# Kernel tuning notes

Hardware: AMD Instinct MI355X
Metric: run time of the kernel (lower is better)

Reference implementation:

```python
import jax, jax.numpy as jnp
import numpy as np

B, T, H, POOL, MAX_ITER = 32, 1024, 128, 16, 4
D = 2 * H  # feature size of U rows


def _maxout(x, w, b, out_dim, pool):
    # x: [..., fin], w: [fin, out_dim*pool], b: [out_dim*pool]
    y = x @ w + b
    y = y.reshape(y.shape[:-1] + (out_dim, pool))
    return y.max(axis=-1)


def _hmn(U, us, ue, h, WDw, WDb, W1w, W1b, W2w, W2b, W3w, W3b):
    # U: [B,T,2H]; us, ue: [B,2H]; h: [B,H] -> scores [B,T]
    r = jnp.tanh(jnp.concatenate([h, us, ue], axis=-1) @ WDw + WDb)  # [B,H]
    rt = jnp.broadcast_to(r[:, None, :], (U.shape[0], U.shape[1], r.shape[-1]))
    m1 = _maxout(jnp.concatenate([U, rt], axis=-1), W1w, W1b, H, POOL)  # [B,T,H]
    m2 = _maxout(m1, W2w, W2b, H, POOL)                                  # [B,T,H]
    m3 = _maxout(jnp.concatenate([m1, m2], axis=-1), W3w, W3b, 1, POOL)  # [B,T,1]
    return m3[..., 0]  # [B,T]


def _lstm_cell(x, h, c, wih, whh, bih, bhh):
    gates = x @ wih.T + bih + h @ whh.T + bhh  # [B,4H]
    i, f, g, o = jnp.split(gates, 4, axis=-1)
    i, f, o = jax.nn.sigmoid(i), jax.nn.sigmoid(f), jax.nn.sigmoid(o)
    g = jnp.tanh(g)
    c2 = f * c + i * g
    h2 = o * jnp.tanh(c2)
    return h2, c2


def setup_inputs() -> dict:
    key = jax.random.key(0)
    ks = jax.random.split(key, 24)
    s = 0.05
    gn = lambda k, shape: (jax.random.normal(k, shape, jnp.float32) * s)
    inp = {"U": jax.random.normal(ks[0], (B, T, D), jnp.float32)}
    for tag, off in (("s", 1), ("e", 9)):
        inp[f"WD{tag}_w"] = gn(ks[off + 0], (5 * H, H))
        inp[f"WD{tag}_b"] = jnp.zeros((H,), jnp.float32)
        inp[f"W1{tag}_w"] = gn(ks[off + 1], (3 * H, H * POOL))
        inp[f"W1{tag}_b"] = jnp.zeros((H * POOL,), jnp.float32)
        inp[f"W2{tag}_w"] = gn(ks[off + 2], (H, H * POOL))
        inp[f"W2{tag}_b"] = jnp.zeros((H * POOL,), jnp.float32)
        inp[f"W3{tag}_w"] = gn(ks[off + 3], (2 * H, POOL))
        inp[f"W3{tag}_b"] = jnp.zeros((POOL,), jnp.float32)
    inp["lstm_wih"] = gn(ks[20], (4 * H, 4 * H))
    inp["lstm_whh"] = gn(ks[21], (4 * H, H))
    inp["lstm_bih"] = jnp.zeros((4 * H,), jnp.float32)
    inp["lstm_bhh"] = jnp.zeros((4 * H,), jnp.float32)
    return inp


def reference(U,
              WDs_w, WDs_b, W1s_w, W1s_b, W2s_w, W2s_b, W3s_w, W3s_b,
              WDe_w, WDe_b, W1e_w, W1e_b, W2e_w, W2e_b, W3e_w, W3e_b,
              lstm_wih, lstm_whh, lstm_bih, lstm_bhh):
    b = U.shape[0]
    bidx = jnp.arange(b)
    h = jnp.zeros((b, H), U.dtype)
    c = jnp.zeros((b, H), U.dtype)
    us, ue = U[:, 0, :], U[:, 1, :]
    entropies = []
    for _ in range(MAX_ITER):  # training-mode: run all iterations (no host-sync early stop)
        alpha_sc = _hmn(U, us, ue, h, WDs_w, WDs_b, W1s_w, W1s_b, W2s_w, W2s_b, W3s_w, W3s_b)
        alpha = jnp.argmax(alpha_sc, axis=1)           # [B]
        us = U[bidx, alpha, :]                          # data-dependent gather
        beta_sc = _hmn(U, us, ue, h, WDe_w, WDe_b, W1e_w, W1e_b, W2e_w, W2e_b, W3e_w, W3e_b)
        beta = jnp.argmax(beta_sc, axis=1)
        ue = U[bidx, beta, :]
        h, c = _lstm_cell(jnp.concatenate([us, ue], axis=1), h, c,
                          lstm_wih, lstm_whh, lstm_bih, lstm_bhh)
        entropies.append(jnp.stack([alpha_sc, beta_sc], axis=0))
    ent = jnp.stack(entropies, axis=0)  # [max_iter, 2, B, T]
    return alpha, beta, ent
```

## Files before the change

### kernel.cpp

```cpp
#include <hip/hip_runtime.h>
#include <math.h>

static constexpr int cB = 32;
static constexpr int cT = 1024;
static constexpr int cH = 128;
static constexpr int cD = 256;
static constexpr int cN = 2048;
static constexpr int cM = cB * cT;

typedef __attribute__((ext_vector_type(8))) short short8;
typedef __attribute__((ext_vector_type(4))) float f32x4;

__device__ __forceinline__ ushort f2bf(float x) {
    union { float f; unsigned u; } v; v.f = x;
    unsigned r = v.u + 0x7FFF + ((v.u >> 16) & 1);
    return (ushort)(r >> 16);
}
__device__ __forceinline__ float bf2f(ushort h) {
    union { float f; unsigned u; } v; v.u = ((unsigned)h) << 16;
    return v.f;
}

__device__ __forceinline__ void gload_lds16(const ushort* g, ushort* l) {
    __builtin_amdgcn_global_load_lds(
        (const __attribute__((address_space(1))) unsigned int*)(const void*)g,
        (__attribute__((address_space(3))) unsigned int*)(void*)l,
        16, 0, 0);
}

template<int K, bool WRITE_HL>
__global__ __launch_bounds__(256, 2)
void mfma_pool_swp(const ushort* __restrict__ Wth, const ushort* __restrict__ Wtl,
                   const ushort* __restrict__ Xh, const ushort* __restrict__ Xl,
                   const float* __restrict__ initv, int init_bstride,
                   float* __restrict__ out, ushort* __restrict__ outh,
                   ushort* __restrict__ outl)
{
    constexpr int KH = K / 128;
    __shared__ __attribute__((aligned(16))) ushort sWh[128 * 128];
    __shared__ __attribute__((aligned(16))) ushort sWl[128 * 128];

    const int tid  = threadIdx.x;
    const int wave = tid >> 6;
    const int lane = tid & 63;
    const int l15  = lane & 15;
    const int lg   = lane >> 4;
    const int wr   = wave >> 1;
    const int wc   = wave & 1;

    const int wg  = blockIdx.x;
    const int lin = (wg & 7) * 512 + (wg >> 3);
    const int bx  = lin & 15;
    const int by  = lin >> 4;
    const int n0  = bx * 128;
    const int m0  = by * 128;
    const size_t ibase = (size_t)(m0 >> 10) * init_bstride;

    float ivv[4][4];
    #pragma unroll
    for (int rf = 0; rf < 4; ++rf)
        #pragma unroll
        for (int r = 0; r < 4; ++r)
            ivv[rf][r] = initv[ibase + n0 + wr * 64 + rf * 16 + lg * 4 + r];

    f32x4 acc[4][4];
    #pragma unroll
    for (int rf = 0; rf < 4; ++rf)
        #pragma unroll
        for (int cf = 0; cf < 4; ++cf)
            acc[rf][cf] = (f32x4){0.f, 0.f, 0.f, 0.f};

    const int st_row_lo = lane >> 4;
    const int st_slot   = lane & 15;

    #pragma unroll
    for (int kh = 0; kh < KH; ++kh) {
        const int kb = kh * 128;
        if (kh > 0) __syncthreads();

        #pragma unroll
        for (int j = 0; j < 8; ++j) {
            int i   = wave * 8 + j;
            int row = i * 4 + st_row_lo;
            int ck  = st_slot ^ (row & 7);
            size_t goff = (size_t)(n0 + row) * K + kb + ck * 8;
            gload_lds16(Wth + goff, sWh + i * 512);
            gload_lds16(Wtl + goff, sWl + i * 512);
        }
        short8 xh_[16], xl_[16];
        #pragma unroll
        for (int cf = 0; cf < 4; ++cf)
            #pragma unroll
            for (int ks = 0; ks < 4; ++ks) {
                size_t off = (size_t)(m0 + wc * 64 + cf * 16 + l15) * K
                           + kb + ks * 32 + lg * 8;
                xh_[cf * 4 + ks] = *(const short8*)(Xh + off);
                xl_[cf * 4 + ks] = *(const short8*)(Xl + off);
            }
        __syncthreads();

        #pragma unroll
        for (int ks = 0; ks < 4; ++ks) {
            short8 w_h[4], w_l[4];
            #pragma unroll
            for (int rf = 0; rf < 4; ++rf) {
                int row  = wr * 64 + rf * 16 + l15;
                int ck2  = ks * 4 + lg;
                int adr  = row * 128 + ((ck2 ^ (row & 7)) * 8);
                w_h[rf] = *(const short8*)(sWh + adr);
                w_l[rf] = *(const short8*)(sWl + adr);
            }
            #pragma unroll
            for (int rf = 0; rf < 4; ++rf)
                #pragma unroll
                for (int cf = 0; cf < 4; ++cf) {
                    acc[rf][cf] = __builtin_amdgcn_mfma_f32_16x16x32_bf16(
                        w_h[rf], xh_[cf * 4 + ks], acc[rf][cf], 0, 0, 0);
                    acc[rf][cf] = __builtin_amdgcn_mfma_f32_16x16x32_bf16(
                        w_l[rf], xh_[cf * 4 + ks], acc[rf][cf], 0, 0, 0);
                    acc[rf][cf] = __builtin_amdgcn_mfma_f32_16x16x32_bf16(
                        w_h[rf], xl_[cf * 4 + ks], acc[rf][cf], 0, 0, 0);
                }
        }
    }

    const int NP = 128;
    #pragma unroll
    for (int rf = 0; rf < 4; ++rf) {
        const int o2 = (n0 >> 4) + wr * 4 + rf;
        #pragma unroll
        for (int cf = 0; cf < 4; ++cf) {
            float v0 = acc[rf][cf][0] + ivv[rf][0];
            float v1 = acc[rf][cf][1] + ivv[rf][1];
            float v2 = acc[rf][cf][2] + ivv[rf][2];
            float v3 = acc[rf][cf][3] + ivv[rf][3];
            float mx = fmaxf(fmaxf(v0, v1), fmaxf(v2, v3));
            mx = fmaxf(mx, __shfl_xor(mx, 16));
            mx = fmaxf(mx, __shfl_xor(mx, 32));
            if (lane < 16) {
                int m = m0 + wc * 64 + cf * 16 + lane;
                size_t o = (size_t)m * NP + o2;
                out[o] = mx;
                if (WRITE_HL) {
                    ushort hb = f2bf(mx);
                    outh[o] = hb;
                    outl[o] = f2bf(mx - bf2f(hb));
                }
            }
        }
    }
}

__global__ __launch_bounds__(256, 2)
void mfma_gemm_a1(const ushort* __restrict__ Uh, const ushort* __restrict__ Ul,
                  const ushort* __restrict__ Bth, const ushort* __restrict__ Btl,
                  float* __restrict__ out)
{
    constexpr int K = 256;
    __shared__ __attribute__((aligned(16))) ushort sBh[128 * 128];
    __shared__ __attribute__((aligned(16))) ushort sBl[128 * 128];

    const int tid  = threadIdx.x;
    const int wave = tid >> 6;
    const int lane = tid & 63;
    const int l15  = lane & 15;
    const int lg   = lane >> 4;
    const int wr   = wave >> 1;
    const int wc   = wave & 1;

    const int wg  = blockIdx.x;
    const int lin = (wg & 7) * 512 + (wg >> 3);
    const int bx  = lin & 15;
    const int by  = lin >> 4;
    const int n0  = bx * 128;
    const int m0  = by * 128;

    f32x4 acc[4][4];
    #pragma unroll
    for (int mf = 0; mf < 4; ++mf)
        #pragma unroll
        for (int nf = 0; nf < 4; ++nf)
            acc[mf][nf] = (f32x4){0.f, 0.f, 0.f, 0.f};

    const int st_row_lo = lane >> 4;
    const int st_slot   = lane & 15;

    #pragma unroll
    for (int kh = 0; kh < 2; ++kh) {
        const int kb = kh * 128;
        if (kh > 0) __syncthreads();

        #pragma unroll
        for (int j = 0; j < 8; ++j) {
            int i   = wave * 8 + j;
            int row = i * 4 + st_row_lo;
            int ck  = st_slot ^ (row & 7);
            size_t goff = (size_t)(n0 + row) * K + kb + ck * 8;
            gload_lds16(Bth + goff, sBh + i * 512);
            gload_lds16(Btl + goff, sBl + i * 512);
        }
        short8 ph[16], pl[16];
        #pragma unroll
        for (int mf = 0; mf < 4; ++mf)
            #pragma unroll
            for (int ks = 0; ks < 4; ++ks) {
                size_t off = (size_t)(m0 + wr * 64 + mf * 16 + l15) * K
                           + kb + ks * 32 + lg * 8;
                ph[mf * 4 + ks] = *(const short8*)(Uh + off);
                pl[mf * 4 + ks] = *(const short8*)(Ul + off);
            }
        __syncthreads();

        #pragma unroll
        for (int ks = 0; ks < 4; ++ks) {
            short8 b_h[4], b_l[4];
            #pragma unroll
            for (int nf = 0; nf < 4; ++nf) {
                int row  = wc * 64 + nf * 16 + l15;
                int ck2  = ks * 4 + lg;
                int adr  = row * 128 + ((ck2 ^ (row & 7)) * 8);
                b_h[nf] = *(const short8*)(sBh + adr);
                b_l[nf] = *(const short8*)(sBl + adr);
            }
            #pragma unroll
            for (int mf = 0; mf < 4; ++mf)
                #pragma unroll
                for (int nf = 0; nf < 4; ++nf) {
                    acc[mf][nf] = __builtin_amdgcn_mfma_f32_16x16x32_bf16(
                        ph[mf * 4 + ks], b_h[nf], acc[mf][nf], 0, 0, 0);
                    acc[mf][nf] = __builtin_amdgcn_mfma_f32_16x16x32_bf16(
                        ph[mf * 4 + ks], b_l[nf], acc[mf][nf], 0, 0, 0);
                    acc[mf][nf] = __builtin_amdgcn_mfma_f32_16x16x32_bf16(
                        pl[mf * 4 + ks], b_h[nf], acc[mf][nf], 0, 0, 0);
                }
        }
    }

    #pragma unroll
    for (int mf = 0; mf < 4; ++mf)
        #pragma unroll
        for (int nf = 0; nf < 4; ++nf) {
            int col = n0 + wc * 64 + nf * 16 + l15;
            #pragma unroll
            for (int r = 0; r < 4; ++r) {
                int row = m0 + wr * 64 + mf * 16 + lg * 4 + r;
                out[(size_t)row * cN + col] = acc[mf][nf][r];
            }
        }
}

__global__ void m1_from_a1_kernel(const float* __restrict__ A1,
                                  const float* __restrict__ rterm,
                                  float* __restrict__ m1,
                                  ushort* __restrict__ m1h,
                                  ushort* __restrict__ m1l)
{
    int idx = blockIdx.x * 256 + threadIdx.x;
    int m = idx >> 7;
    int o = idx & 127;
    int b = m >> 10;
    const float4* a  = (const float4*)(A1 + (size_t)m * cN + o * 16);
    const float4* rt = (const float4*)(rterm + (size_t)b * cN + o * 16);
    float mx = -3.4e38f;
    #pragma unroll
    for (int q = 0; q < 4; ++q) {
        float4 av = a[q];
        float4 rv = rt[q];
        mx = fmaxf(mx, fmaxf(fmaxf(av.x + rv.x, av.y + rv.y),
                             fmaxf(av.z + rv.z, av.w + rv.w)));
    }
    m1[idx] = mx;
    ushort hb = f2bf(mx);
    m1h[idx] = hb;
    m1l[idx] = f2bf(mx - bf2f(hb));
}

__global__ void wsplit_kernel(const float* __restrict__ W, int K, int N,
                              ushort* __restrict__ th, ushort* __restrict__ tl)
{
    int idx = blockIdx.x * 256 + threadIdx.x;
    if (idx >= K * N) return;
    int k = idx / N, n = idx - k * N;
    float x = W[idx];
    ushort h = f2bf(x);
    th[(size_t)n * K + k] = h;
    tl[(size_t)n * K + k] = f2bf(x - bf2f(h));
}

__global__ void usplit_kernel(const float* __restrict__ U,
                              ushort* __restrict__ uh, ushort* __restrict__ ul)
{
    int idx = blockIdx.x * 256 + threadIdx.x;
    float x = U[idx];
    ushort h = f2bf(x);
    uh[idx] = h;
    ul[idx] = f2bf(x - bf2f(h));
}

__global__ void r_kernel(const float* __restrict__ h, const float* __restrict__ us,
                         const float* __restrict__ ue,
                         const float* __restrict__ WDw, const float* __restrict__ WDb,
                         float* __restrict__ r)
{
    int b = blockIdx.x;
    int j = threadIdx.x;
    __shared__ float x[640];
    x[j]       = h[b * cH + j];
    x[128 + j] = us[b * cD + j];
    x[256 + j] = us[b * cD + 128 + j];
    x[384 + j] = ue[b * cD + j];
    x[512 + j] = ue[b * cD + 128 + j];
    __syncthreads();
    float s = WDb[j];
    for (int k = 0; k < 640; ++k) s = fmaf(x[k], WDw[(size_t)k * cH + j], s);
    r[b * cH + j] = tanhf(s);
}

__global__ void rterm_kernel(const float* __restrict__ r, const float* __restrict__ W1r,
                             const float* __restrict__ W1b, float* __restrict__ rterm)
{
    int b = blockIdx.y;
    int n = blockIdx.x * 256 + threadIdx.x;
    __shared__ float rs[128];
    if (threadIdx.x < 128) rs[threadIdx.x] = r[b * cH + threadIdx.x];
    __syncthreads();
    float s = W1b[n];
    for (int k = 0; k < 128; ++k) s = fmaf(rs[k], W1r[(size_t)k * cN + n], s);
    rterm[(size_t)b * cN + n] = s;
}

__global__ __launch_bounds__(256)
void score_kernel(const float* __restrict__ m1, const float* __restrict__ m2,
                  const float* __restrict__ W3w, const float* __restrict__ W3b,
                  float* __restrict__ ent)
{
    __shared__ float xs[16][257];
    __shared__ float wsh[256 * 16];
    int tid = threadIdx.x;
    int m0 = blockIdx.x * 16;
    #pragma unroll
    for (int q = 0; q < 16; ++q) wsh[tid + q * 256] = W3w[tid + q * 256];
    #pragma unroll
    for (int q = 0; q < 8; ++q) {
        int f = tid + q * 256;
        int rl = f >> 7, col = f & 127;
        xs[rl][col]       = m1[(size_t)(m0 + rl) * cH + col];
        xs[rl][128 + col] = m2[(size_t)(m0 + rl) * cH + col];
    }
    __syncthreads();
    int rl = tid >> 4, p = tid & 15;
    float s = W3b[p];
    for (int k = 0; k < 256; ++k) s = fmaf(xs[rl][k], wsh[k * 16 + p], s);
    #pragma unroll
    for (int off = 8; off; off >>= 1) s = fmaxf(s, __shfl_xor(s, off));
    if (p == 0) ent[m0 + rl] = s;
}

__global__ void argmax_kernel(const float* __restrict__ sc, const float* __restrict__ U,
                              float* __restrict__ uvec, float* __restrict__ outidx)
{
    int b = blockIdx.x;
    int tid = threadIdx.x;
    float bv = -3.4e38f;
    int bi = 0x7fffffff;
    for (int t = tid; t < cT; t += 256) {
        float v = sc[b * cT + t];
        if (v > bv || (v == bv && t < bi)) { bv = v; bi = t; }
    }
    __shared__ float vs[256];
    __shared__ int   is[256];
    vs[tid] = bv; is[tid] = bi;
    __syncthreads();
    for (int s = 128; s > 0; s >>= 1) {
        if (tid < s) {
            if (vs[tid + s] > vs[tid] ||
                (vs[tid + s] == vs[tid] && is[tid + s] < is[tid])) {
                vs[tid] = vs[tid + s];
                is[tid] = is[tid + s];
            }
        }
        __syncthreads();
    }
    int best = is[0];
    if (tid == 0) outidx[b] = (float)best;
    uvec[b * cD + tid % cD] = U[((size_t)b * cT + best) * cD + (tid % cD)];
}

__global__ void lstm_kernel(const float* __restrict__ us, const float* __restrict__ ue,
                            float* __restrict__ h, float* __restrict__ c,
                            const float* __restrict__ wih, const float* __restrict__ whh,
                            const float* __restrict__ bih, const float* __restrict__ bhh)
{
    int b = blockIdx.x;
    int j = threadIdx.x;
    __shared__ float x[512];
    __shared__ float hh[128];
    x[j]       = us[b * cD + j];
    x[128 + j] = us[b * cD + 128 + j];
    x[256 + j] = ue[b * cD + j];
    x[384 + j] = ue[b * cD + 128 + j];
    hh[j] = h[b * cH + j];
    __syncthreads();
    float g4[4];
    #pragma unroll
    for (int gi = 0; gi < 4; ++gi) {
        int row = gi * 128 + j;
        float s = bih[row] + bhh[row];
        const float* wr = wih + (size_t)row * 512;
        for (int k = 0; k < 512; ++k) s = fmaf(x[k], wr[k], s);
        const float* wr2 = whh + (size_t)row * 128;
        for (int k = 0; k < 128; ++k) s = fmaf(hh[k], wr2[k], s);
        g4[gi] = s;
    }
    float i_ = 1.f / (1.f + expf(-g4[0]));
    float f_ = 1.f / (1.f + expf(-g4[1]));
    float g_ = tanhf(g4[2]);
    float o_ = 1.f / (1.f + expf(-g4[3]));
    float c2 = f_ * c[b * cH + j] + i_ * g_;
    float h2 = o_ * tanhf(c2);
    c[b * cH + j] = c2;
    h[b * cH + j] = h2;
}

__global__ void init_kernel(const float* __restrict__ U, float* __restrict__ us,
                            float* __restrict__ ue, float* __restrict__ h,
                            float* __restrict__ c)
{
    int i = blockIdx.x * 256 + threadIdx.x;
    if (i < cB * cD) {
        int b = i >> 8, d = i & 255;
        us[i] = U[((size_t)b * cT + 0) * cD + d];
        ue[i] = U[((size_t)b * cT + 1) * cD + d];
    }
    if (i < cB * cH) { h[i] = 0.f; c[i] = 0.f; }
}

extern "C" void kernel_launch(void* const* d_in, const int* in_sizes, int n_in,
                              void* d_out, int out_size, void* d_ws, size_t ws_size,
                              hipStream_t stream)
{
    const float* U = (const float*)d_in[0];
    const float* WD_w[2] = {(const float*)d_in[1], (const float*)d_in[9]};
    const float* WD_b[2] = {(const float*)d_in[2], (const float*)d_in[10]};
    const float* W1_w[2] = {(const float*)d_in[3], (const float*)d_in[11]};
    const float* W1_b[2] = {(const float*)d_in[4], (const float*)d_in[12]};
    const float* W2_w[2] = {(const float*)d_in[5], (const float*)d_in[13]};
    const float* W2_b[2] = {(const float*)d_in[6], (const float*)d_in[14]};
    const float* W3_w[2] = {(const float*)d_in[7], (const float*)d_in[15]};
    const float* W3_b[2] = {(const float*)d_in[8], (const float*)d_in[16]};
    const float* wih = (const float*)d_in[17];
    const float* whh = (const float*)d_in[18];
    const float* bih = (const float*)d_in[19];
    const float* bhh = (const float*)d_in[20];

    float* ws = (float*)d_ws;
    float* m1 = ws;
    float* m2 = m1 + (size_t)cM * cH;
    float* us = m2 + (size_t)cM * cH;
    float* ue = us + cB * cD;
    float* h  = ue + cB * cD;
    float* c  = h + cB * cH;
    float* r  = c + cB * cH;
    float* rterm = r + cB * cH;
    float* cur = rterm + (size_t)cB * cN;

    ushort* m1h = (ushort*)cur;                   cur += (size_t)cM * cH / 2;
    ushort* m1l = (ushort*)cur;                   cur += (size_t)cM * cH / 2;
    ushort* Uh  = (ushort*)cur;                   cur += (size_t)cM * cD / 2;
    ushort* Ul  = (ushort*)cur;                   cur += (size_t)cM * cD / 2;
    ushort* W1th[2], *W1tl[2], *W2th[2], *W2tl[2];
    for (int sd = 0; sd < 2; ++sd) {
        W1th[sd] = (ushort*)cur; cur += (size_t)cN * cD / 2;
        W1tl[sd] = (ushort*)cur; cur += (size_t)cN * cD / 2;
        W2th[sd] = (ushort*)cur; cur += (size_t)cN * cH / 2;
        W2tl[sd] = (ushort*)cur; cur += (size_t)cN * cH / 2;
    }
    float* A1[2];
    A1[0] = cur;
    A1[1] = A1[0] + (size_t)cM * cN;
    size_t need = (size_t)(A1[1] - ws) + (size_t)cM * cN;
    bool pre = ws_size >= need * sizeof(float);

    float* outf = (float*)d_out;

    init_kernel<<<32, 256, 0, stream>>>(U, us, ue, h, c);
    usplit_kernel<<<(cM * cD) / 256, 256, 0, stream>>>(U, Uh, Ul);
    for (int sd = 0; sd < 2; ++sd) {
        wsplit_kernel<<<(cD * cN) / 256, 256, 0, stream>>>(
            W1_w[sd], cD, cN, W1th[sd], W1tl[sd]);
        wsplit_kernel<<<(cH * cN) / 256, 256, 0, stream>>>(
            W2_w[sd], cH, cN, W2th[sd], W2tl[sd]);
    }

    const int ggrid = (cN / 128) * (cM / 128);
    if (pre) {
        for (int sd = 0; sd < 2; ++sd)
            mfma_gemm_a1<<<ggrid, 256, 0, stream>>>(
                Uh, Ul, W1th[sd], W1tl[sd], A1[sd]);
    }

    for (int it = 0; it < 4; ++it) {
        for (int sd = 0; sd < 2; ++sd) {
            r_kernel<<<32, 128, 0, stream>>>(h, us, ue, WD_w[sd], WD_b[sd], r);
            rterm_kernel<<<dim3(8, 32), 256, 0, stream>>>(
                r, W1_w[sd] + (size_t)256 * cN, W1_b[sd], rterm);
            if (pre) {
                m1_from_a1_kernel<<<16384, 256, 0, stream>>>(
                    A1[sd], rterm, m1, m1h, m1l);
            } else {
                mfma_pool_swp<256, true><<<ggrid, 256, 0, stream>>>(
                    W1th[sd], W1tl[sd], Uh, Ul, rterm, cN, m1, m1h, m1l);
            }
            mfma_pool_swp<128, false><<<ggrid, 256, 0, stream>>>(
                W2th[sd], W2tl[sd], m1h, m1l, W2_b[sd], 0, m2, nullptr, nullptr);
            float* ent = outf + 64 + (size_t)(it * 2 + sd) * cB * cT;
            score_kernel<<<2048, 256, 0, stream>>>(m1, m2, W3_w[sd], W3_b[sd], ent);
            argmax_kernel<<<32, 256, 0, stream>>>(ent, U, sd ? ue : us,
                                                  outf + (sd ? 32 : 0));
        }
        lstm_kernel<<<32, 128, 0, stream>>>(us, ue, h, c, wih, whh, bih, bhh);
    }
}
```

Baseline: 2.868 ms.

## Use weight-stationary persistent MFMA kernels for A1 precompute and W2 maxout GEMM

Replaces the LDS-staged A1 GEMM and the per-iteration W2 maxout GEMM with weight-stationary kernels. Each workgroup keeps its slice of the split bf16 weights in registers and loops over many M sub-tiles, streaming activations straight from global memory. The grid shrinks to 256 workgroups, which removes repeated LDS staging of the weights and the syncs around it. In exchange it raises register pressure (launch bounds 1), gives less parallelism and latency hiding, and loads activations without LDS reuse across waves.

```diff
diff --git a/kernel.cpp b/kernel.cpp
--- a/kernel.cpp
+++ b/kernel.cpp
@@ -26,6 +26,179 @@
         (const __attribute__((address_space(1))) unsigned int*)(const void*)g,
         (__attribute__((address_space(3))) unsigned int*)(void*)l,
         16, 0, 0);
+}
+
+__global__ __launch_bounds__(256, 1)
+void mfma_pool_ws(const ushort* __restrict__ Wth, const ushort* __restrict__ Wtl,
+                  const ushort* __restrict__ Xh, const ushort* __restrict__ Xl,
+                  const float* __restrict__ bias, float* __restrict__ out)
+{
+    constexpr int K = 128;
+    const int lane = threadIdx.x & 63;
+    const int wave = threadIdx.x >> 6;
+    const int l15  = lane & 15;
+    const int lg   = lane >> 4;
+    const int wr   = wave >> 1;
+    const int wc   = wave & 1;
+
+    const int wg  = blockIdx.x;
+    const int lin = (wg & 7) * 32 + (wg >> 3);
+    const int bx  = lin & 15;
+    const int by  = lin >> 4;
+    const int n0  = bx * 128;
+    const int mg0 = by * 2048;
+
+    short8 w_h[4][4], w_l[4][4];
+    #pragma unroll
+    for (int rf = 0; rf < 4; ++rf)
+        #pragma unroll
+        for (int ks = 0; ks < 4; ++ks) {
+            size_t off = (size_t)(n0 + wr * 64 + rf * 16 + l15) * K
+                       + ks * 32 + lg * 8;
+            w_h[rf][ks] = *(const short8*)(Wth + off);
+            w_l[rf][ks] = *(const short8*)(Wtl + off);
+        }
+    float ivv[4][4];
+    #pragma unroll
+    for (int rf = 0; rf < 4; ++rf)
+        #pragma unroll
+        for (int r = 0; r < 4; ++r)
+            ivv[rf][r] = bias[n0 + wr * 64 + rf * 16 + lg * 4 + r];
+
+    const int NP = 128;
+    #pragma unroll 1
+    for (int sub = 0; sub < 16; ++sub) {
+        const int m0 = mg0 + sub * 128;
+
+        short8 xh_[4][4], xl_[4][4];
+        #pragma unroll
+        for (int cf = 0; cf < 4; ++cf)
+            #pragma unroll
+            for (int ks = 0; ks < 4; ++ks) {
+                size_t off = (size_t)(m0 + wc * 64 + cf * 16 + l15) * K
+                           + ks * 32 + lg * 8;
+                xh_[cf][ks] = *(const short8*)(Xh + off);
+                xl_[cf][ks] = *(const short8*)(Xl + off);
+            }
+
+        f32x4 acc[4][4];
+        #pragma unroll
+        for (int rf = 0; rf < 4; ++rf)
+            #pragma unroll
+            for (int cf = 0; cf < 4; ++cf)
+                acc[rf][cf] = (f32x4){0.f, 0.f, 0.f, 0.f};
+
+        #pragma unroll
+        for (int ks = 0; ks < 4; ++ks)
+            #pragma unroll
+            for (int rf = 0; rf < 4; ++rf)
+                #pragma unroll
+                for (int cf = 0; cf < 4; ++cf) {
+                    acc[rf][cf] = __builtin_amdgcn_mfma_f32_16x16x32_bf16(
+                        w_h[rf][ks], xh_[cf][ks], acc[rf][cf], 0, 0, 0);
+                    acc[rf][cf] = __builtin_amdgcn_mfma_f32_16x16x32_bf16(
+                        w_l[rf][ks], xh_[cf][ks], acc[rf][cf], 0, 0, 0);
+                    acc[rf][cf] = __builtin_amdgcn_mfma_f32_16x16x32_bf16(
+                        w_h[rf][ks], xl_[cf][ks], acc[rf][cf], 0, 0, 0);
+                }
+
+        #pragma unroll
+        for (int rf = 0; rf < 4; ++rf) {
+            const int o2 = (n0 >> 4) + wr * 4 + rf;
+            #pragma unroll
+            for (int cf = 0; cf < 4; ++cf) {
+                float v0 = acc[rf][cf][0] + ivv[rf][0];
+                float v1 = acc[rf][cf][1] + ivv[rf][1];
+                float v2 = acc[rf][cf][2] + ivv[rf][2];
+                float v3 = acc[rf][cf][3] + ivv[rf][3];
+                float mx = fmaxf(fmaxf(v0, v1), fmaxf(v2, v3));
+                mx = fmaxf(mx, __shfl_xor(mx, 16));
+                mx = fmaxf(mx, __shfl_xor(mx, 32));
+                if (lane < 16) {
+                    int m = m0 + wc * 64 + cf * 16 + lane;
+                    out[(size_t)m * NP + o2] = mx;
+                }
+            }
+        }
+    }
+}
+
+__global__ __launch_bounds__(256, 1)
+void mfma_a1_ws(const ushort* __restrict__ Uh, const ushort* __restrict__ Ul,
+                const ushort* __restrict__ Bth, const ushort* __restrict__ Btl,
+                float* __restrict__ out)
+{
+    constexpr int K = 256;
+    const int lane = threadIdx.x & 63;
+    const int wave = threadIdx.x >> 6;
+    const int l15  = lane & 15;
+    const int lg   = lane >> 4;
+    const int wr   = wave >> 1;
+    const int wc   = wave & 1;
+
+    const int wg  = blockIdx.x;
+    const int lin = (wg & 7) * 32 + (wg >> 3);
+    const int bx  = lin & 31;
+    const int by  = lin >> 5;
+    const int n0  = bx * 64;
+    const int mg0 = by * 4096;
+
+    short8 b_h[2][8], b_l[2][8];
+    #pragma unroll
+    for (int nf = 0; nf < 2; ++nf)
+        #pragma unroll
+        for (int ks = 0; ks < 8; ++ks) {
+            size_t off = (size_t)(n0 + wc * 32 + nf * 16 + l15) * K
+                       + ks * 32 + lg * 8;
+            b_h[nf][ks] = *(const short8*)(Bth + off);
+            b_l[nf][ks] = *(const short8*)(Btl + off);
+        }
+
+    #pragma unroll 1
+    for (int sub = 0; sub < 32; ++sub) {
+        const int m0 = mg0 + sub * 128;
+        f32x4 acc[4][2];
+        #pragma unroll
+        for (int mf = 0; mf < 4; ++mf)
+            #pragma unroll
+            for (int nf = 0; nf < 2; ++nf)
+                acc[mf][nf] = (f32x4){0.f, 0.f, 0.f, 0.f};
+
+        #pragma unroll
+        for (int mf = 0; mf < 4; ++mf) {
+            short8 uh_[8], ul_[8];
+            #pragma unroll
+            for (int ks = 0; ks < 8; ++ks) {
+                size_t off = (size_t)(m0 + wr * 64 + mf * 16 + l15) * K
+                           + ks * 32 + lg * 8;
+                uh_[ks] = *(const short8*)(Uh + off);
+                ul_[ks] = *(const short8*)(Ul + off);
+            }
+            #pragma unroll
+            for (int ks = 0; ks < 8; ++ks)
+                #pragma unroll
+                for (int nf = 0; nf < 2; ++nf) {
+                    acc[mf][nf] = __builtin_amdgcn_mfma_f32_16x16x32_bf16(
+                        uh_[ks], b_h[nf][ks], acc[mf][nf], 0, 0, 0);
+                    acc[mf][nf] = __builtin_amdgcn_mfma_f32_16x16x32_bf16(
+                        uh_[ks], b_l[nf][ks], acc[mf][nf], 0, 0, 0);
+                    acc[mf][nf] = __builtin_amdgcn_mfma_f32_16x16x32_bf16(
+                        ul_[ks], b_h[nf][ks], acc[mf][nf], 0, 0, 0);
+                }
+        }
+
+        #pragma unroll
+        for (int mf = 0; mf < 4; ++mf)
+            #pragma unroll
+            for (int nf = 0; nf < 2; ++nf) {
+                int col = n0 + wc * 32 + nf * 16 + l15;
+                #pragma unroll
+                for (int r = 0; r < 4; ++r) {
+                    int row = m0 + wr * 64 + mf * 16 + lg * 4 + r;
+                    out[(size_t)row * cN + col] = acc[mf][nf][r];
+                }
+            }
+    }
 }
 
 template<int K, bool WRITE_HL>
@@ -151,104 +324,6 @@
     }
 }
 
-__global__ __launch_bounds__(256, 2)
-void mfma_gemm_a1(const ushort* __restrict__ Uh, const ushort* __restrict__ Ul,
-                  const ushort* __restrict__ Bth, const ushort* __restrict__ Btl,
-                  float* __restrict__ out)
-{
-    constexpr int K = 256;
-    __shared__ __attribute__((aligned(16))) ushort sBh[128 * 128];
-    __shared__ __attribute__((aligned(16))) ushort sBl[128 * 128];
-
-    const int tid  = threadIdx.x;
-    const int wave = tid >> 6;
-    const int lane = tid & 63;
-    const int l15  = lane & 15;
-    const int lg   = lane >> 4;
-    const int wr   = wave >> 1;
-    const int wc   = wave & 1;
-
-    const int wg  = blockIdx.x;
-    const int lin = (wg & 7) * 512 + (wg >> 3);
-    const int bx  = lin & 15;
-    const int by  = lin >> 4;
-    const int n0  = bx * 128;
-    const int m0  = by * 128;
-
-    f32x4 acc[4][4];
-    #pragma unroll
-    for (int mf = 0; mf < 4; ++mf)
-        #pragma unroll
-        for (int nf = 0; nf < 4; ++nf)
-            acc[mf][nf] = (f32x4){0.f, 0.f, 0.f, 0.f};
-
-    const int st_row_lo = lane >> 4;
-    const int st_slot   = lane & 15;
-
-    #pragma unroll
-    for (int kh = 0; kh < 2; ++kh) {
-        const int kb = kh * 128;
-        if (kh > 0) __syncthreads();
-
-        #pragma unroll
-        for (int j = 0; j < 8; ++j) {
-            int i   = wave * 8 + j;
-            int row = i * 4 + st_row_lo;
-            int ck  = st_slot ^ (row & 7);
-            size_t goff = (size_t)(n0 + row) * K + kb + ck * 8;
-            gload_lds16(Bth + goff, sBh + i * 512);
-            gload_lds16(Btl + goff, sBl + i * 512);
-        }
-        short8 ph[16], pl[16];
-        #pragma unroll
-        for (int mf = 0; mf < 4; ++mf)
-            #pragma unroll
-            for (int ks = 0; ks < 4; ++ks) {
-                size_t off = (size_t)(m0 + wr * 64 + mf * 16 + l15) * K
-                           + kb + ks * 32 + lg * 8;
-                ph[mf * 4 + ks] = *(const short8*)(Uh + off);
-                pl[mf * 4 + ks] = *(const short8*)(Ul + off);
-            }
-        __syncthreads();
-
-        #pragma unroll
-        for (int ks = 0; ks < 4; ++ks) {
-            short8 b_h[4], b_l[4];
-            #pragma unroll
-            for (int nf = 0; nf < 4; ++nf) {
-                int row  = wc * 64 + nf * 16 + l15;
-                int ck2  = ks * 4 + lg;
-                int adr  = row * 128 + ((ck2 ^ (row & 7)) * 8);
-                b_h[nf] = *(const short8*)(sBh + adr);
-                b_l[nf] = *(const short8*)(sBl + adr);
-            }
-            #pragma unroll
-            for (int mf = 0; mf < 4; ++mf)
-                #pragma unroll
-                for (int nf = 0; nf < 4; ++nf) {
-                    acc[mf][nf] = __builtin_amdgcn_mfma_f32_16x16x32_bf16(
-                        ph[mf * 4 + ks], b_h[nf], acc[mf][nf], 0, 0, 0);
-                    acc[mf][nf] = __builtin_amdgcn_mfma_f32_16x16x32_bf16(
-                        ph[mf * 4 + ks], b_l[nf], acc[mf][nf], 0, 0, 0);
-                    acc[mf][nf] = __builtin_amdgcn_mfma_f32_16x16x32_bf16(
-                        pl[mf * 4 + ks], b_h[nf], acc[mf][nf], 0, 0, 0);
-                }
-        }
-    }
-
-    #pragma unroll
-    for (int mf = 0; mf < 4; ++mf)
-        #pragma unroll
-        for (int nf = 0; nf < 4; ++nf) {
-            int col = n0 + wc * 64 + nf * 16 + l15;
-            #pragma unroll
-            for (int r = 0; r < 4; ++r) {
-                int row = m0 + wr * 64 + mf * 16 + lg * 4 + r;
-                out[(size_t)row * cN + col] = acc[mf][nf][r];
-            }
-        }
-}
-
 __global__ void m1_from_a1_kernel(const float* __restrict__ A1,
                                   const float* __restrict__ rterm,
                                   float* __restrict__ m1,
@@ -492,13 +567,13 @@
             W2_w[sd], cH, cN, W2th[sd], W2tl[sd]);
     }
 
-    const int ggrid = (cN / 128) * (cM / 128);
     if (pre) {
         for (int sd = 0; sd < 2; ++sd)
-            mfma_gemm_a1<<<ggrid, 256, 0, stream>>>(
+            mfma_a1_ws<<<256, 256, 0, stream>>>(
                 Uh, Ul, W1th[sd], W1tl[sd], A1[sd]);
     }
 
+    const int gfall = (cN / 128) * (cM / 128);
     for (int it = 0; it < 4; ++it) {
         for (int sd = 0; sd < 2; ++sd) {
             r_kernel<<<32, 128, 0, stream>>>(h, us, ue, WD_w[sd], WD_b[sd], r);
@@ -508,11 +583,11 @@
                 m1_from_a1_kernel<<<16384, 256, 0, stream>>>(
                     A1[sd], rterm, m1, m1h, m1l);
             } else {
-                mfma_pool_swp<256, true><<<ggrid, 256, 0, stream>>>(
+                mfma_pool_swp<256, true><<<gfall, 256, 0, stream>>>(
                     W1th[sd], W1tl[sd], Uh, Ul, rterm, cN, m1, m1h, m1l);
             }
-            mfma_pool_swp<128, false><<<ggrid, 256, 0, stream>>>(
-                W2th[sd], W2tl[sd], m1h, m1l, W2_b[sd], 0, m2, nullptr, nullptr);
+            mfma_pool_ws<<<256, 256, 0, stream>>>(
+                W2th[sd], W2tl[sd], m1h, m1l, W2_b[sd], m2);
             float* ent = outf + 64 + (size_t)(it * 2 + sd) * cB * cT;
             score_kernel<<<2048, 256, 0, stream>>>(m1, m2, W3_w[sd], W3_b[sd], ent);
             argmax_kernel<<<32, 256, 0, stream>>>(ent, U, sd ? ue : us,
```

Measured after the change: 3.198 ms. 1.12x slower.

## Partially precompute A1 to fit workspace and persist W2 tiles across M blocks

Applied to the files above, without the earlier changes.

Replaces the all-or-nothing precompute of U@W1 with a split: as many rows as fit in the workspace are precomputed once, and the remainder run through the fused MFMA pool kernel at an M offset. Adds a dedicated m2 kernel that loads the W2 tile into LDS once and loops over four 128-row M blocks, cutting redundant weight staging and halving the grid. The m2 kernel also uses three MFMAs, dropping the low-low bf16 product, which slightly reduces precision.

```diff
diff --git a/kernel.cpp b/kernel.cpp
--- a/kernel.cpp
+++ b/kernel.cpp
@@ -28,15 +28,14 @@
         16, 0, 0);
 }
 
-template<int K, bool WRITE_HL>
 __global__ __launch_bounds__(256, 2)
 void mfma_pool_swp(const ushort* __restrict__ Wth, const ushort* __restrict__ Wtl,
                    const ushort* __restrict__ Xh, const ushort* __restrict__ Xl,
                    const float* __restrict__ initv, int init_bstride,
                    float* __restrict__ out, ushort* __restrict__ outh,
-                   ushort* __restrict__ outl)
-{
-    constexpr int KH = K / 128;
+                   ushort* __restrict__ outl, int mOff, int gridDiv8)
+{
+    constexpr int K = 256;
     __shared__ __attribute__((aligned(16))) ushort sWh[128 * 128];
     __shared__ __attribute__((aligned(16))) ushort sWl[128 * 128];
 
@@ -49,11 +48,11 @@
     const int wc   = wave & 1;
 
     const int wg  = blockIdx.x;
-    const int lin = (wg & 7) * 512 + (wg >> 3);
+    const int lin = (wg & 7) * gridDiv8 + (wg >> 3);
     const int bx  = lin & 15;
     const int by  = lin >> 4;
     const int n0  = bx * 128;
-    const int m0  = by * 128;
+    const int m0  = mOff + by * 128;
     const size_t ibase = (size_t)(m0 >> 10) * init_bstride;
 
     float ivv[4][4];
@@ -74,7 +73,7 @@
     const int st_slot   = lane & 15;
 
     #pragma unroll
-    for (int kh = 0; kh < KH; ++kh) {
+    for (int kh = 0; kh < 2; ++kh) {
         const int kb = kh * 128;
         if (kh > 0) __syncthreads();
 
@@ -141,11 +140,9 @@
                 int m = m0 + wc * 64 + cf * 16 + lane;
                 size_t o = (size_t)m * NP + o2;
                 out[o] = mx;
-                if (WRITE_HL) {
-                    ushort hb = f2bf(mx);
-                    outh[o] = hb;
-                    outl[o] = f2bf(mx - bf2f(hb));
-                }
+                ushort hb = f2bf(mx);
+                outh[o] = hb;
+                outl[o] = f2bf(mx - bf2f(hb));
             }
         }
     }
@@ -154,7 +151,7 @@
 __global__ __launch_bounds__(256, 2)
 void mfma_gemm_a1(const ushort* __restrict__ Uh, const ushort* __restrict__ Ul,
                   const ushort* __restrict__ Bth, const ushort* __restrict__ Btl,
-                  float* __restrict__ out)
+                  float* __restrict__ out, int gridDiv8)
 {
     constexpr int K = 256;
     __shared__ __attribute__((aligned(16))) ushort sBh[128 * 128];
@@ -169,7 +166,7 @@
     const int wc   = wave & 1;
 
     const int wg  = blockIdx.x;
-    const int lin = (wg & 7) * 512 + (wg >> 3);
+    const int lin = (wg & 7) * gridDiv8 + (wg >> 3);
     const int bx  = lin & 15;
     const int by  = lin >> 4;
     const int n0  = bx * 128;
@@ -273,6 +270,117 @@
     ushort hb = f2bf(mx);
     m1h[idx] = hb;
     m1l[idx] = f2bf(mx - bf2f(hb));
+}
+
+__global__ __launch_bounds__(256, 2)
+void mfma_pool_m2(const ushort* __restrict__ Wth, const ushort* __restrict__ Wtl,
+                  const ushort* __restrict__ Xh, const ushort* __restrict__ Xl,
+                  const float* __restrict__ bias, float* __restrict__ out)
+{
+    constexpr int K = 128;
+    __shared__ __attribute__((aligned(16))) ushort sWh[128 * 128];
+    __shared__ __attribute__((aligned(16))) ushort sWl[128 * 128];
+
+    const int tid  = threadIdx.x;
+    const int wave = tid >> 6;
+    const int lane = tid & 63;
+    const int l15  = lane & 15;
+    const int lg   = lane >> 4;
+    const int wr   = wave >> 1;
+    const int wc   = wave & 1;
+
+    const int wg  = blockIdx.x;
+    const int lin = (wg & 7) * 128 + (wg >> 3);
+    const int bx  = lin & 15;
+    const int by  = lin >> 4;
+    const int n0  = bx * 128;
+
+    float ivv[4][4];
+    #pragma unroll
+    for (int rf = 0; rf < 4; ++rf)
+        #pragma unroll
+        for (int r = 0; r < 4; ++r)
+            ivv[rf][r] = bias[n0 + wr * 64 + rf * 16 + lg * 4 + r];
+
+    const int st_row_lo = lane >> 4;
+    const int st_slot   = lane & 15;
+    #pragma unroll
+    for (int j = 0; j < 8; ++j) {
+        int i   = wave * 8 + j;
+        int row = i * 4 + st_row_lo;
+        int ck  = st_slot ^ (row & 7);
+        size_t goff = (size_t)(n0 + row) * K + ck * 8;
+        gload_lds16(Wth + goff, sWh + i * 512);
+        gload_lds16(Wtl + goff, sWl + i * 512);
+    }
+    __syncthreads();
+
+    const int NP = 128;
+    #pragma unroll 1
+    for (int s = 0; s < 4; ++s) {
+        const int m0 = by * 512 + s * 128;
+
+        short8 xh_[16], xl_[16];
+        #pragma unroll
+        for (int cf = 0; cf < 4; ++cf)
+            #pragma unroll
+            for (int ks = 0; ks < 4; ++ks) {
+                size_t off = (size_t)(m0 + wc * 64 + cf * 16 + l15) * K
+                           + ks * 32 + lg * 8;
+                xh_[cf * 4 + ks] = *(const short8*)(Xh + off);
+                xl_[cf * 4 + ks] = *(const short8*)(Xl + off);
+            }
+
+        f32x4 acc[4][4];
+        #pragma unroll
+        for (int rf = 0; rf < 4; ++rf)
+            #pragma unroll
+            for (int cf = 0; cf < 4; ++cf)
+                acc[rf][cf] = (f32x4){0.f, 0.f, 0.f, 0.f};
+
+        #pragma unroll
+        for (int ks = 0; ks < 4; ++ks) {
+            short8 w_h[4], w_l[4];
+            #pragma unroll
+            for (int rf = 0; rf < 4; ++rf) {
+                int row  = wr * 64 + rf * 16 + l15;
+                int ck2  = ks * 4 + lg;
+                int adr  = row * 128 + ((ck2 ^ (row & 7)) * 8);
+                w_h[rf] = *(const short8*)(sWh + adr);
+                w_l[rf] = *(const short8*)(sWl + adr);
+            }
+            #pragma unroll
+            for (int rf = 0; rf < 4; ++rf)
+                #pragma unroll
+                for (int cf = 0; cf < 4; ++cf) {
+                    acc[rf][cf] = __builtin_amdgcn_mfma_f32_16x16x32_bf16(
+                        w_h[rf], xh_[cf * 4 + ks], acc[rf][cf], 0, 0, 0);
+                    acc[rf][cf] = __builtin_amdgcn_mfma_f32_16x16x32_bf16(
+                        w_l[rf], xh_[cf * 4 + ks], acc[rf][cf], 0, 0, 0);
+                    acc[rf][cf] = __builtin_amdgcn_mfma_f32_16x16x32_bf16(
+                        w_h[rf], xl_[cf * 4 + ks], acc[rf][cf], 0, 0, 0);
+                }
+        }
+
+        #pragma unroll
+        for (int rf = 0; rf < 4; ++rf) {
+            const int o2 = (n0 >> 4) + wr * 4 + rf;
+            #pragma unroll
+            for (int cf = 0; cf < 4; ++cf) {
+                float v0 = acc[rf][cf][0] + ivv[rf][0];
+                float v1 = acc[rf][cf][1] + ivv[rf][1];
+                float v2 = acc[rf][cf][2] + ivv[rf][2];
+                float v3 = acc[rf][cf][3] + ivv[rf][3];
+                float mx = fmaxf(fmaxf(v0, v1), fmaxf(v2, v3));
+                mx = fmaxf(mx, __shfl_xor(mx, 16));
+                mx = fmaxf(mx, __shfl_xor(mx, 32));
+                if (lane < 16) {
+                    int m = m0 + wc * 64 + cf * 16 + lane;
+                    out[(size_t)m * NP + o2] = mx;
+                }
+            }
+        }
+    }
 }
 
 __global__ void wsplit_kernel(const float* __restrict__ W, int K, int N,
@@ -475,11 +583,17 @@
         W2th[sd] = (ushort*)cur; cur += (size_t)cN * cH / 2;
         W2tl[sd] = (ushort*)cur; cur += (size_t)cN * cH / 2;
     }
+
+    size_t baseBytes = (size_t)((char*)cur - (char*)ws);
+    size_t rowBytes  = (size_t)cN * sizeof(float);
+    size_t availRows = ws_size > baseBytes ? (ws_size - baseBytes) / rowBytes : 0;
+    int a1r[2];
+    a1r[0] = (int)((availRows > (size_t)cM ? (size_t)cM : availRows) & ~(size_t)127);
+    size_t rem = availRows - (size_t)a1r[0];
+    a1r[1] = (int)((rem > (size_t)cM ? (size_t)cM : rem) & ~(size_t)127);
     float* A1[2];
-    A1[0] = cur;
-    A1[1] = A1[0] + (size_t)cM * cN;
-    size_t need = (size_t)(A1[1] - ws) + (size_t)cM * cN;
-    bool pre = ws_size >= need * sizeof(float);
+    A1[0] = (float*)cur;
+    A1[1] = A1[0] + (size_t)a1r[0] * cN;
 
     float* outf = (float*)d_out;
 
@@ -492,27 +606,29 @@
             W2_w[sd], cH, cN, W2th[sd], W2tl[sd]);
     }
 
-    const int ggrid = (cN / 128) * (cM / 128);
-    if (pre) {
-        for (int sd = 0; sd < 2; ++sd)
-            mfma_gemm_a1<<<ggrid, 256, 0, stream>>>(
-                Uh, Ul, W1th[sd], W1tl[sd], A1[sd]);
-    }
+    for (int sd = 0; sd < 2; ++sd)
+        if (a1r[sd] > 0) {
+            int mB = a1r[sd] / 128;
+            mfma_gemm_a1<<<16 * mB, 256, 0, stream>>>(
+                Uh, Ul, W1th[sd], W1tl[sd], A1[sd], 2 * mB);
+        }
 
     for (int it = 0; it < 4; ++it) {
         for (int sd = 0; sd < 2; ++sd) {
             r_kernel<<<32, 128, 0, stream>>>(h, us, ue, WD_w[sd], WD_b[sd], r);
             rterm_kernel<<<dim3(8, 32), 256, 0, stream>>>(
                 r, W1_w[sd] + (size_t)256 * cN, W1_b[sd], rterm);
-            if (pre) {
-                m1_from_a1_kernel<<<16384, 256, 0, stream>>>(
+            if (a1r[sd] > 0)
+                m1_from_a1_kernel<<<a1r[sd] / 2, 256, 0, stream>>>(
                     A1[sd], rterm, m1, m1h, m1l);
-            } else {
-                mfma_pool_swp<256, true><<<ggrid, 256, 0, stream>>>(
-                    W1th[sd], W1tl[sd], Uh, Ul, rterm, cN, m1, m1h, m1l);
-            }
-            mfma_pool_swp<128, false><<<ggrid, 256, 0, stream>>>(
-                W2th[sd], W2tl[sd], m1h, m1l, W2_b[sd], 0, m2, nullptr, nullptr);
+            if (a1r[sd] < cM) {
+                int mB = (cM - a1r[sd]) / 128;
+                mfma_pool_swp<<<16 * mB, 256, 0, stream>>>(
+                    W1th[sd], W1tl[sd], Uh, Ul, rterm, cN, m1, m1h, m1l,
+                    a1r[sd], 2 * mB);
+            }
+            mfma_pool_m2<<<1024, 256, 0, stream>>>(
+                W2th[sd], W2tl[sd], m1h, m1l, W2_b[sd], m2);
             float* ent = outf + 64 + (size_t)(it * 2 + sd) * cB * cT;
             score_kernel<<<2048, 256, 0, stream>>>(m1, m2, W3_w[sd], W3_b[sd], ent);
             argmax_kernel<<<32, 256, 0, stream>>>(ent, U, sd ? ue : us,
```

Measured after the change: 2.923 ms. No clear change (+1.9%).
